# Kernel tuning notes

Hardware: AMD Instinct MI355X
Metric: run time of the kernel (lower is better)

## Reference

```python
import jax, jax.numpy as jnp
import numpy as np

B, S, HS = 2, 2048, 2048
H, HKV, D = 16, 4, 128
EPS = 1e-6
NEG = -1e9


def _rms_norm(t, w):
    t32 = t.astype(jnp.float32)
    n = t32 * jax.lax.rsqrt(jnp.mean(t32 * t32, axis=-1, keepdims=True) + EPS)
    return (w.astype(t.dtype) * n.astype(t.dtype))


def _rotate_half(x):
    x1, x2 = jnp.split(x, 2, axis=-1)
    return jnp.concatenate((-x2, x1), axis=-1)


def setup_inputs() -> dict:
    key = jax.random.key(0)
    ks = jax.random.split(key, 6)
    x = jax.random.normal(ks[0], (B, S, HS), dtype=jnp.float32)
    # RoPE tables
    inv_freq = 1.0 / (10000.0 ** (jnp.arange(0, D, 2, dtype=jnp.float32) / D))
    freqs = jnp.arange(S, dtype=jnp.float32)[:, None] * inv_freq[None, :]  # [S, D/2]
    emb = jnp.concatenate((freqs, freqs), axis=-1)  # [S, D]
    cos, sin = jnp.cos(emb), jnp.sin(emb)
    # causal additive mask [1,1,S,S]
    mask = jnp.triu(jnp.full((S, S), NEG, dtype=jnp.float32), k=1)[None, None]
    std = 0.02
    wq = jax.random.normal(ks[1], (H * D, HS), dtype=jnp.float32) * std
    wk = jax.random.normal(ks[2], (HKV * D, HS), dtype=jnp.float32) * std
    wv = jax.random.normal(ks[3], (HKV * D, HS), dtype=jnp.float32) * std
    wo = jax.random.normal(ks[4], (HS, H * D), dtype=jnp.float32) * std
    q_norm_w = jnp.ones((D,), dtype=jnp.float32)
    k_norm_w = jnp.ones((D,), dtype=jnp.float32)
    return {"x": x, "cos": cos, "sin": sin, "mask": mask,
            "wq": wq, "wk": wk, "wv": wv, "wo": wo,
            "q_norm_w": q_norm_w, "k_norm_w": k_norm_w}


def reference(x, cos, sin, mask, wq, wk, wv, wo, q_norm_w, k_norm_w):
    b, s, _ = x.shape
    n_rep = H // HKV
    scale = D ** -0.5
    # QKV projections (torch Linear: y = x @ W^T)
    q = jnp.einsum('bsh,oh->bso', x, wq).reshape(b, s, H, D).transpose(0, 2, 1, 3)
    k = jnp.einsum('bsh,oh->bso', x, wk).reshape(b, s, HKV, D).transpose(0, 2, 1, 3)
    v = jnp.einsum('bsh,oh->bso', x, wv).reshape(b, s, HKV, D).transpose(0, 2, 1, 3)
    # per-head RMS QK-norm
    q = _rms_norm(q, q_norm_w)
    k = _rms_norm(k, k_norm_w)
    # RoPE
    c = cos[None, None]
    sn = sin[None, None]
    q = q * c + _rotate_half(q) * sn
    k = k * c + _rotate_half(k) * sn
    # GQA attention without materializing repeated K/V
    qg = q.reshape(b, HKV, n_rep, s, D)
    scores = jnp.einsum('bhgqd,bhkd->bhgqk', qg, k) * scale + mask  # [b,HKV,G,S,S]
    probs = jax.nn.softmax(scores, axis=-1)
    out = jnp.einsum('bhgqk,bhkd->bhgqd', probs, v)  # [b,HKV,G,S,D]
    out = out.reshape(b, H, s, D).transpose(0, 2, 1, 3).reshape(b, s, H * D)
    return jnp.einsum('bso,ho->bsh', out, wo)
```

## Files before the change

### kernel.cpp

```cpp
#include <hip/hip_runtime.h>
#include <hip/hip_bf16.h>
#include <stdint.h>

typedef unsigned short u16;
typedef __attribute__((ext_vector_type(8))) short short8;
typedef __attribute__((ext_vector_type(4))) float f32x4;
typedef __attribute__((ext_vector_type(4))) unsigned short u16x4;

constexpr int BB = 2, SS = 2048, HSZ = 2048, NH = 16, NKV = 4, DH = 128;
constexpr int MROWS = BB * SS;
constexpr int NQKV = (NH + 2 * NKV) * DH;
constexpr float RMS_EPS = 1e-6f;

__device__ __forceinline__ u16 f2bf(float f) {
  __hip_bfloat16 h = __float2bfloat16(f);
  return *reinterpret_cast<u16*>(&h);
}
__device__ __forceinline__ float bf2f(u16 u) {
  __hip_bfloat16 h;
  *reinterpret_cast<u16*>(&h) = u;
  return __bfloat162float(h);
}

__device__ __forceinline__ void gld16(const void* g, void* l) {
  __builtin_amdgcn_global_load_lds(
      (const __attribute__((address_space(1))) void*)g,
      (__attribute__((address_space(3))) void*)l, 16, 0, 0);
}

__global__ void cvt_bf16_kernel(const float* __restrict__ in, u16* __restrict__ out, int n4) {
  int i = blockIdx.x * blockDim.x + threadIdx.x;
  if (i >= n4) return;
  float4 v = reinterpret_cast<const float4*>(in)[i];
  u16x4 o;
  o.x = f2bf(v.x); o.y = f2bf(v.y); o.z = f2bf(v.z); o.w = f2bf(v.w);
  reinterpret_cast<u16x4*>(out)[i] = o;
}

template <typename OutT>
__global__ __launch_bounds__(512, 2) void gemm256(
    const u16* __restrict__ A, const u16* __restrict__ Bm, OutT* __restrict__ C,
    int M, int N, int K, int nbn) {
  __shared__ u16 Abuf[4][256 * 32];
  __shared__ u16 Bbuf[4][256 * 32];
  const int tid = threadIdx.x;
  const int wave = tid >> 6;
  const int lane = tid & 63;
  const int nwg = gridDim.x;
  const int bid = blockIdx.x;
  const int wg = (bid & 7) * (nwg >> 3) + (bid >> 3);
  const int bm = wg / nbn, bn = wg % nbn;
  const int row0 = bm * 256, col0 = bn * 256;
  const int wm = wave >> 2, wn = wave & 3;
  const int lr = lane & 15, g = lane >> 4;
  const int sra = wave * 16 + (lane >> 2);
  const int sca = (lane & 3) * 8;
  const int lda0 = (wave * 16) * 32;
  const int lda1 = (128 + wave * 16) * 32;

  f32x4 acc[8][4] = {};
  const int nt = K / 32;

#define STAGE(T, BUFI)                                                        \
  {                                                                           \
    const int k0_ = (T) * 32;                                                 \
    u16* Ab_ = &Abuf[(BUFI)][0];                                              \
    u16* Bb_ = &Bbuf[(BUFI)][0];                                              \
    gld16(A + (size_t)(row0 + sra) * K + k0_ + sca, Ab_ + lda0);              \
    gld16(A + (size_t)(row0 + 128 + sra) * K + k0_ + sca, Ab_ + lda1);        \
    gld16(Bm + (size_t)(col0 + sra) * K + k0_ + sca, Bb_ + lda0);             \
    gld16(Bm + (size_t)(col0 + 128 + sra) * K + k0_ + sca, Bb_ + lda1);       \
  }

  STAGE(0, 0);
  STAGE(1, 1);

  for (int t = 0; t < nt; t++) {
    if (t + 2 < nt) {
      STAGE(t + 2, (t + 2) & 3);
      asm volatile("s_waitcnt vmcnt(8)" ::: "memory");
    } else if (t + 1 < nt) {
      asm volatile("s_waitcnt vmcnt(4)" ::: "memory");
    } else {
      asm volatile("s_waitcnt vmcnt(0)" ::: "memory");
    }
    __builtin_amdgcn_s_barrier();
    __builtin_amdgcn_sched_barrier(0);

    const u16* Ab = &Abuf[t & 3][0];
    const u16* Bb = &Bbuf[t & 3][0];
    short8 af[8], bfr[4];
#pragma unroll
    for (int m = 0; m < 8; m++)
      af[m] = *(const short8*)&Ab[(wm * 128 + m * 16 + lr) * 32 + g * 8];
#pragma unroll
    for (int n = 0; n < 4; n++)
      bfr[n] = *(const short8*)&Bb[(wn * 64 + n * 16 + lr) * 32 + g * 8];

    __builtin_amdgcn_s_setprio(1);
#pragma unroll
    for (int m = 0; m < 8; m++)
#pragma unroll
      for (int n = 0; n < 4; n++)
        acc[m][n] = __builtin_amdgcn_mfma_f32_16x16x32_bf16(af[m], bfr[n], acc[m][n], 0, 0, 0);
    __builtin_amdgcn_s_setprio(0);

    __builtin_amdgcn_s_barrier();
    __builtin_amdgcn_sched_barrier(0);
  }
#undef STAGE

  const int cr = g * 4, cc = lr;
#pragma unroll
  for (int m = 0; m < 8; m++) {
#pragma unroll
    for (int n = 0; n < 4; n++) {
#pragma unroll
      for (int r = 0; r < 4; r++) {
        size_t idx = (size_t)(row0 + wm * 128 + m * 16 + cr + r) * N +
                     (col0 + wn * 64 + n * 16 + cc);
        if constexpr (sizeof(OutT) == 2) C[idx] = (OutT)f2bf(acc[m][n][r]);
        else C[idx] = acc[m][n][r];
      }
    }
  }
}

__global__ __launch_bounds__(256) void postproc_kernel(
    const u16* __restrict__ Cqkv, const float* __restrict__ cosT,
    const float* __restrict__ sinT, const float* __restrict__ qw,
    const float* __restrict__ kw, u16* __restrict__ qO, u16* __restrict__ kO,
    u16* __restrict__ vO) {
  const int row = blockIdx.x;
  const int b = row / SS, s = row % SS;
  const int wave = threadIdx.x >> 6, lane = threadIdx.x & 63;
  const u16* base = Cqkv + (size_t)row * NQKV;
  const int d0 = lane * 2;
  const float ATT_SCALE = 0.08838834764831843f * 1.4426950408889634f;
  for (int hd = wave; hd < NH + 2 * NKV; hd += 4) {
    const u16* hp = base + hd * DH;
    ushort2 raw = *(const ushort2*)(hp + d0);
    if (hd < NH + NKV) {
      float v0 = bf2f(raw.x), v1 = bf2f(raw.y);
      float ss = v0 * v0 + v1 * v1;
#pragma unroll
      for (int off = 32; off > 0; off >>= 1) ss += __shfl_xor(ss, off);
      float inv = rsqrtf(ss * (1.0f / DH) + RMS_EPS);
      const float* w = (hd < NH) ? qw : kw;
      float n0 = v0 * inv * w[d0], n1 = v1 * inv * w[d0 + 1];
      float r0 = __shfl_xor(n0, 32), r1 = __shfl_xor(n1, 32);
      float sgn = (lane < 32) ? -1.f : 1.f;
      float c0 = cosT[s * DH + d0], c1 = cosT[s * DH + d0 + 1];
      float s0 = sinT[s * DH + d0], s1 = sinT[s * DH + d0 + 1];
      float o0 = n0 * c0 + sgn * r0 * s0;
      float o1 = n1 * c1 + sgn * r1 * s1;
      ushort2 o;
      if (hd < NH) {
        o.x = f2bf(o0 * ATT_SCALE);
        o.y = f2bf(o1 * ATT_SCALE);
        *(ushort2*)(qO + ((size_t)((b * NH + hd) * SS + s)) * DH + d0) = o;
      } else {
        o.x = f2bf(o0);
        o.y = f2bf(o1);
        *(ushort2*)(kO + ((size_t)((b * NKV + hd - NH) * SS + s)) * DH + d0) = o;
      }
    } else {
      *(ushort2*)(vO + ((size_t)((b * NKV + hd - NH - NKV) * SS + s)) * DH + d0) = raw;
    }
  }
}

__global__ __launch_bounds__(256) void transpose_v_kernel(const u16* __restrict__ v,
                                                          u16* __restrict__ vt) {
  __shared__ u16 tile[64][68];
  const int bh = blockIdx.z;
  const int st = blockIdx.x * 64;
  const int dt = blockIdx.y * 64;
  const int tid = threadIdx.x;
  const u16* src = v + ((size_t)bh * SS + st) * DH + dt;
#pragma unroll
  for (int it = 0; it < 4; it++) {
    int r = (tid >> 4) + it * 16, c = (tid & 15) * 4;
    *(u16x4*)&tile[r][c] = *(const u16x4*)(src + (size_t)r * DH + c);
  }
  __syncthreads();
  u16* dst = vt + ((size_t)bh * DH + dt) * SS + st;
#pragma unroll
  for (int it = 0; it < 4; it++) {
    int r2 = (tid >> 4) + it * 16, c2 = (tid & 15) * 4;
    u16x4 o;
    o.x = tile[c2][r2]; o.y = tile[c2 + 1][r2];
    o.z = tile[c2 + 2][r2]; o.w = tile[c2 + 3][r2];
    *(u16x4*)(dst + (size_t)r2 * SS + c2) = o;
  }
}

__global__ __launch_bounds__(256, 2) void attn_kernel(
    const u16* __restrict__ Q, const u16* __restrict__ Kb,
    const u16* __restrict__ Vt, u16* __restrict__ O) {
  __shared__ __align__(16) u16 Ks[64 * 128];
  __shared__ __align__(16) u16 Vs[128 * 64];
  __shared__ __align__(16) u16 Plds[4][16 * 64];
  const int pid = blockIdx.x, h = blockIdx.y, b = blockIdx.z;
  const int hkv = h >> 2;
  const int tid = threadIdx.x;
  const int wave = tid >> 6, lane = tid & 63;
  const int lr = lane & 15, g = lane >> 4;
  const u16* qbase = Q + ((size_t)(b * NH + h) * SS) * DH;
  const u16* kbase = Kb + ((size_t)(b * NKV + hkv) * SS) * DH;
  const u16* vbase = Vt + ((size_t)(b * NKV + hkv) * DH) * SS;

  const int krow = tid >> 4;
  const int kcol = (tid & 15) * 8;
  const int kswz = kcol ^ ((krow & 7) << 3);
  const int vrow = tid >> 3;
  const int vcol = (tid & 7) * 8;
  const int vswz = vcol ^ ((vrow & 7) << 3);
  const int kx = (lr & 7) << 3;
  const int psw = (lr & 7) << 4;
  char* pl = (char*)&Plds[wave][0];

  int4 kr0, kr1, kr2, kr3, vr0, vr1, vr2, vr3;
#define STAGE_LOAD(T)                                                         \
  {                                                                           \
    const int kv0_ = (T) * 64;                                                \
    kr0 = *(const int4*)(kbase + (size_t)(kv0_ + krow) * DH + kcol);          \
    kr1 = *(const int4*)(kbase + (size_t)(kv0_ + krow + 16) * DH + kcol);     \
    kr2 = *(const int4*)(kbase + (size_t)(kv0_ + krow + 32) * DH + kcol);     \
    kr3 = *(const int4*)(kbase + (size_t)(kv0_ + krow + 48) * DH + kcol);     \
    vr0 = *(const int4*)(vbase + (size_t)(vrow) * SS + kv0_ + vcol);          \
    vr1 = *(const int4*)(vbase + (size_t)(vrow + 32) * SS + kv0_ + vcol);     \
    vr2 = *(const int4*)(vbase + (size_t)(vrow + 64) * SS + kv0_ + vcol);     \
    vr3 = *(const int4*)(vbase + (size_t)(vrow + 96) * SS + kv0_ + vcol);     \
  }
#define STAGE_WRITE()                                                         \
  {                                                                           \
    *(int4*)&Ks[(krow) * DH + kswz] = kr0;                                    \
    *(int4*)&Ks[(krow + 16) * DH + kswz] = kr1;                               \
    *(int4*)&Ks[(krow + 32) * DH + kswz] = kr2;                               \
    *(int4*)&Ks[(krow + 48) * DH + kswz] = kr3;                               \
    *(int4*)&Vs[(vrow) * 64 + vswz] = vr0;                                    \
    *(int4*)&Vs[(vrow + 32) * 64 + vswz] = vr1;                               \
    *(int4*)&Vs[(vrow + 64) * 64 + vswz] = vr2;                               \
    *(int4*)&Vs[(vrow + 96) * 64 + vswz] = vr3;                               \
  }

#pragma unroll 1
  for (int half = 0; half < 2; half++) {
    const int qt = half ? (SS / 64 - 1 - pid) : pid;
    const int q0 = qt * 64 + wave * 16;
    const int nt = qt + 1;

    short8 qf[4];
#pragma unroll
    for (int c = 0; c < 4; c++)
      qf[c] = *(const short8*)(qbase + (size_t)(q0 + lr) * DH + c * 32 + g * 8);

    f32x4 o_acc[8] = {};
    float l_run = 0.f;

    STAGE_LOAD(0);
    STAGE_WRITE();
    __syncthreads();

    for (int t = 0; t < nt; t++) {
      const int kv0 = t * 64;
      if (t + 1 < nt) STAGE_LOAD(t + 1);

      f32x4 sf[4] = {};
      __builtin_amdgcn_s_setprio(1);
#pragma unroll
      for (int n = 0; n < 4; n++) {
#pragma unroll
        for (int c = 0; c < 4; c++) {
          short8 kf = *(const short8*)&Ks[(n * 16 + lr) * DH + ((c * 32 + g * 8) ^ kx)];
          sf[n] = __builtin_amdgcn_mfma_f32_16x16x32_bf16(kf, qf[c], sf[n], 0, 0, 0);
        }
      }
      __builtin_amdgcn_s_setprio(0);

      const int qabs = q0 + lr;
      float p[4][4];
      float rs = 0.f;
#pragma unroll
      for (int n = 0; n < 4; n++) {
#pragma unroll
        for (int r = 0; r < 4; r++) {
          const int kvabs = kv0 + n * 16 + g * 4 + r;
          float e = exp2f(sf[n][r] - 17.312340490667562f);
          e = (kvabs <= qabs) ? e : 0.f;
          p[n][r] = e;
          rs += e;
        }
      }
      rs += __shfl_xor(rs, 16);
      rs += __shfl_xor(rs, 32);
      l_run += rs;

#pragma unroll
      for (int n = 0; n < 4; n++) {
        uint2 wv;
        wv.x = (unsigned)f2bf(p[n][0]) | ((unsigned)f2bf(p[n][1]) << 16);
        wv.y = (unsigned)f2bf(p[n][2]) | ((unsigned)f2bf(p[n][3]) << 16);
        *(uint2*)(pl + lr * 128 + ((32 * n + 8 * g) ^ psw)) = wv;
      }

      __builtin_amdgcn_s_setprio(1);
#pragma unroll
      for (int c2 = 0; c2 < 2; c2++) {
        short8 pf = *(const short8*)(pl + lr * 128 + ((64 * c2 + 16 * g) ^ psw));
#pragma unroll
        for (int n2 = 0; n2 < 8; n2++) {
          short8 vf = *(const short8*)&Vs[(n2 * 16 + lr) * 64 + ((c2 * 32 + g * 8) ^ kx)];
          o_acc[n2] = __builtin_amdgcn_mfma_f32_16x16x32_bf16(pf, vf, o_acc[n2], 0, 0, 0);
        }
      }
      __builtin_amdgcn_s_setprio(0);

      __syncthreads();
      if (t + 1 < nt) STAGE_WRITE();
      __syncthreads();
    }

#pragma unroll
    for (int r = 0; r < 4; r++) {
      const float ls = __shfl(l_run, (g << 4) | (g * 4 + r));
      const float inv = 1.0f / ls;
      u16* orow = O + ((size_t)(b * SS + q0 + g * 4 + r)) * (NH * DH) + h * DH;
#pragma unroll
      for (int n2 = 0; n2 < 8; n2++) orow[n2 * 16 + lr] = f2bf(o_acc[n2][r] * inv);
    }
  }
#undef STAGE_LOAD
#undef STAGE_WRITE
}

extern "C" void kernel_launch(void* const* d_in, const int* in_sizes, int n_in,
                              void* d_out, int out_size, void* d_ws, size_t ws_size,
                              hipStream_t stream) {
  const float* x    = (const float*)d_in[0];
  const float* cosT = (const float*)d_in[1];
  const float* sinT = (const float*)d_in[2];
  const float* wq = (const float*)d_in[4];
  const float* wk = (const float*)d_in[5];
  const float* wv = (const float*)d_in[6];
  const float* wo = (const float*)d_in[7];
  const float* qw = (const float*)d_in[8];
  const float* kw = (const float*)d_in[9];
  float* out = (float*)d_out;

  char* p = (char*)d_ws;
  u16* xb    = (u16*)p; p += (size_t)MROWS * HSZ * 2;
  u16* wqkvb = (u16*)p; p += (size_t)NQKV * HSZ * 2;
  u16* wob   = (u16*)p; p += (size_t)HSZ * HSZ * 2;
  u16* cqkv  = (u16*)p; p += (size_t)MROWS * NQKV * 2;
  u16* qb    = (u16*)p; p += (size_t)BB * NH * SS * DH * 2;
  u16* kb    = (u16*)p; p += (size_t)BB * NKV * SS * DH * 2;
  u16* vb    = (u16*)p; p += (size_t)BB * NKV * SS * DH * 2;
  u16* vtb   = (u16*)p; p += (size_t)BB * NKV * SS * DH * 2;
  u16* aob   = (u16*)p; p += (size_t)MROWS * HSZ * 2;

  auto cvt = [&](const float* in, u16* o, size_t n) {
    int n4 = (int)(n / 4);
    cvt_bf16_kernel<<<dim3((n4 + 255) / 256), dim3(256), 0, stream>>>(in, o, n4);
  };
  cvt(x, xb, (size_t)MROWS * HSZ);
  cvt(wq, wqkvb, (size_t)NH * DH * HSZ);
  cvt(wk, wqkvb + (size_t)NH * DH * HSZ, (size_t)NKV * DH * HSZ);
  cvt(wv, wqkvb + (size_t)(NH + NKV) * DH * HSZ, (size_t)NKV * DH * HSZ);
  cvt(wo, wob, (size_t)HSZ * HSZ);

  gemm256<u16><<<dim3((MROWS / 256) * (NQKV / 256)), dim3(512), 0, stream>>>(
      xb, wqkvb, cqkv, MROWS, NQKV, HSZ, NQKV / 256);
  postproc_kernel<<<dim3(MROWS), dim3(256), 0, stream>>>(cqkv, cosT, sinT, qw, kw, qb, kb, vb);
  transpose_v_kernel<<<dim3(SS / 64, DH / 64, BB * NKV), dim3(256), 0, stream>>>(vb, vtb);
  attn_kernel<<<dim3(SS / 128, NH, BB), dim3(256), 0, stream>>>(qb, kb, vtb, aob);
  gemm256<float><<<dim3((MROWS / 256) * (HSZ / 256)), dim3(512), 0, stream>>>(
      aob, wob, out, MROWS, HSZ, HSZ, HSZ / 256);
}
```

Measured before the change: 396.0 us.

## Restructure GEMM main loop with swizzled LDS and interleaved half-tile staging; fuse conversions

Rewrites the 256x256 GEMM main loop to process two K-tiles per iteration. Each tile's MFMA work is split into two half-tile phases, and the global-to-LDS loads for A and B are interleaved between those phases. LDS rows get an XOR swizzle to avoid bank conflicts on fragment reads, and fewer A fragments are held at once, which lowers register pressure. The five separate fp32->bf16 conversion launches are merged into one kernel to cut launch overhead. In exchange the loop needs more barriers and hand-tuned waitcnt logic that is easy to get subtly wrong.

```diff
diff --git a/kernel.cpp b/kernel.cpp
--- a/kernel.cpp
+++ b/kernel.cpp
@@ -28,87 +28,152 @@
       (__attribute__((address_space(3))) void*)l, 16, 0, 0);
 }
 
-__global__ void cvt_bf16_kernel(const float* __restrict__ in, u16* __restrict__ out, int n4) {
+constexpr int N_X = MROWS * HSZ;
+constexpr int N_WQ = NH * DH * HSZ;
+constexpr int N_WK = NKV * DH * HSZ;
+constexpr int N_WO = HSZ * HSZ;
+__global__ void cvt_all_kernel(const float* __restrict__ x, const float* __restrict__ wq,
+                               const float* __restrict__ wk, const float* __restrict__ wv,
+                               const float* __restrict__ wo, u16* __restrict__ xb,
+                               u16* __restrict__ wqkvb, u16* __restrict__ wob) {
+  const int X4 = N_X / 4, Q4 = N_WQ / 4, K4 = N_WK / 4;
   int i = blockIdx.x * blockDim.x + threadIdx.x;
-  if (i >= n4) return;
-  float4 v = reinterpret_cast<const float4*>(in)[i];
+  const float* src;
+  u16* dst;
+  int off;
+  if (i < X4) { src = x; dst = xb; off = i; }
+  else if (i < X4 + Q4) { src = wq; dst = wqkvb; off = i - X4; }
+  else if (i < X4 + Q4 + K4) { src = wk; dst = wqkvb + N_WQ; off = i - X4 - Q4; }
+  else if (i < X4 + Q4 + 2 * K4) { src = wv; dst = wqkvb + N_WQ + N_WK; off = i - X4 - Q4 - K4; }
+  else { src = wo; dst = wob; off = i - X4 - Q4 - 2 * K4; }
+  float4 v = reinterpret_cast<const float4*>(src)[off];
   u16x4 o;
   o.x = f2bf(v.x); o.y = f2bf(v.y); o.z = f2bf(v.z); o.w = f2bf(v.w);
-  reinterpret_cast<u16x4*>(out)[i] = o;
+  reinterpret_cast<u16x4*>(dst)[off] = o;
 }
 
 template <typename OutT>
 __global__ __launch_bounds__(512, 2) void gemm256(
     const u16* __restrict__ A, const u16* __restrict__ Bm, OutT* __restrict__ C,
     int M, int N, int K, int nbn) {
-  __shared__ u16 Abuf[4][256 * 32];
-  __shared__ u16 Bbuf[4][256 * 32];
+  __shared__ __align__(16) u16 AS[4][256 * 32];
+  __shared__ __align__(16) u16 BS[4][256 * 32];
   const int tid = threadIdx.x;
-  const int wave = tid >> 6;
-  const int lane = tid & 63;
-  const int nwg = gridDim.x;
-  const int bid = blockIdx.x;
+  const int wave = tid >> 6, lane = tid & 63;
+  const int nwg = gridDim.x, bid = blockIdx.x;
   const int wg = (bid & 7) * (nwg >> 3) + (bid >> 3);
   const int bm = wg / nbn, bn = wg % nbn;
   const int row0 = bm * 256, col0 = bn * 256;
   const int wm = wave >> 2, wn = wave & 3;
   const int lr = lane & 15, g = lane >> 4;
-  const int sra = wave * 16 + (lane >> 2);
-  const int sca = (lane & 3) * 8;
-  const int lda0 = (wave * 16) * 32;
-  const int lda1 = (128 + wave * 16) * 32;
+
+  const int rsrc = ((tid >> 5) << 3) | ((tid & 7) ^ ((tid >> 3) & 3));
+  const int sce = ((tid >> 3) & 3) << 3;
+  const int rxor = g * 128 + (((lr & 7) ^ g) << 4);
+  const int abase = (wm * 128) << 6;
+  const int bbase = (wn * 64) << 6;
 
   f32x4 acc[8][4] = {};
-  const int nt = K / 32;
-
-#define STAGE(T, BUFI)                                                        \
-  {                                                                           \
-    const int k0_ = (T) * 32;                                                 \
-    u16* Ab_ = &Abuf[(BUFI)][0];                                              \
-    u16* Bb_ = &Bbuf[(BUFI)][0];                                              \
-    gld16(A + (size_t)(row0 + sra) * K + k0_ + sca, Ab_ + lda0);              \
-    gld16(A + (size_t)(row0 + 128 + sra) * K + k0_ + sca, Ab_ + lda1);        \
-    gld16(Bm + (size_t)(col0 + sra) * K + k0_ + sca, Bb_ + lda0);             \
-    gld16(Bm + (size_t)(col0 + 128 + sra) * K + k0_ + sca, Bb_ + lda1);       \
-  }
-
-  STAGE(0, 0);
-  STAGE(1, 1);
-
-  for (int t = 0; t < nt; t++) {
-    if (t + 2 < nt) {
-      STAGE(t + 2, (t + 2) & 3);
-      asm volatile("s_waitcnt vmcnt(8)" ::: "memory");
-    } else if (t + 1 < nt) {
-      asm volatile("s_waitcnt vmcnt(4)" ::: "memory");
-    } else {
-      asm volatile("s_waitcnt vmcnt(0)" ::: "memory");
-    }
-    __builtin_amdgcn_s_barrier();
+  const int niter = K / 64;
+
+#define STG_A(kt, sl, j)                                                      \
+  gld16(A + (size_t)(row0 + (j) * 128 + rsrc) * K + (kt) * 32 + sce,          \
+        (char*)&AS[sl][0] + (j) * 8192 + wave * 1024)
+#define STG_B(kt, sl, j)                                                      \
+  gld16(Bm + (size_t)(col0 + (j) * 128 + rsrc) * K + (kt) * 32 + sce,         \
+        (char*)&BS[sl][0] + (j) * 8192 + wave * 1024)
+
+  STG_A(0, 0, 0); STG_A(0, 0, 1); STG_B(0, 0, 0); STG_B(0, 0, 1);
+  STG_A(1, 1, 0); STG_A(1, 1, 1); STG_B(1, 1, 0); STG_B(1, 1, 1);
+  asm volatile("s_waitcnt vmcnt(4)" ::: "memory");
+  __builtin_amdgcn_s_barrier();
+
+  for (int it = 0; it < niter; it++) {
+    const bool stg = (it + 1) < niter;
+    const int slA = (2 * it) & 3, slB = (2 * it + 1) & 3;
+    const int ktS = 2 * it + 2;
+    const int ss0 = ktS & 3, ss1 = (ktS + 1) & 3;
+    const char* Ab = (const char*)&AS[slA][0];
+    const char* Bb = (const char*)&BS[slA][0];
+    short8 bf[4], af[4];
+
+#pragma unroll
+    for (int n = 0; n < 4; n++)
+      bf[n] = *(const short8*)(Bb + bbase + ((n * 16 + (lr & 8)) << 6) + rxor);
+#pragma unroll
+    for (int m = 0; m < 4; m++)
+      af[m] = *(const short8*)(Ab + abase + ((m * 16 + (lr & 8)) << 6) + rxor);
+    if (stg) { STG_A(ktS, ss0, 0); STG_A(ktS, ss0, 1); }
+    __builtin_amdgcn_s_barrier();
+    asm volatile("s_waitcnt lgkmcnt(0)" ::: "memory");
     __builtin_amdgcn_sched_barrier(0);
-
-    const u16* Ab = &Abuf[t & 3][0];
-    const u16* Bb = &Bbuf[t & 3][0];
-    short8 af[8], bfr[4];
-#pragma unroll
-    for (int m = 0; m < 8; m++)
-      af[m] = *(const short8*)&Ab[(wm * 128 + m * 16 + lr) * 32 + g * 8];
+    __builtin_amdgcn_s_setprio(1);
+#pragma unroll
+    for (int m = 0; m < 4; m++)
+#pragma unroll
+      for (int n = 0; n < 4; n++)
+        acc[m][n] = __builtin_amdgcn_mfma_f32_16x16x32_bf16(af[m], bf[n], acc[m][n], 0, 0, 0);
+    __builtin_amdgcn_s_setprio(0);
+    __builtin_amdgcn_s_barrier();
+
+#pragma unroll
+    for (int m = 0; m < 4; m++)
+      af[m] = *(const short8*)(Ab + abase + ((64 + m * 16 + (lr & 8)) << 6) + rxor);
+    if (stg) { STG_B(ktS, ss0, 0); STG_B(ktS, ss0, 1); }
+    __builtin_amdgcn_s_barrier();
+    asm volatile("s_waitcnt lgkmcnt(0)" ::: "memory");
+    __builtin_amdgcn_sched_barrier(0);
+    __builtin_amdgcn_s_setprio(1);
+#pragma unroll
+    for (int m = 0; m < 4; m++)
+#pragma unroll
+      for (int n = 0; n < 4; n++)
+        acc[4 + m][n] = __builtin_amdgcn_mfma_f32_16x16x32_bf16(af[m], bf[n], acc[4 + m][n], 0, 0, 0);
+    __builtin_amdgcn_s_setprio(0);
+    if (stg) asm volatile("s_waitcnt vmcnt(4)" ::: "memory");
+    else     asm volatile("s_waitcnt vmcnt(0)" ::: "memory");
+    __builtin_amdgcn_s_barrier();
+
+    Ab = (const char*)&AS[slB][0];
+    Bb = (const char*)&BS[slB][0];
 #pragma unroll
     for (int n = 0; n < 4; n++)
-      bfr[n] = *(const short8*)&Bb[(wn * 64 + n * 16 + lr) * 32 + g * 8];
-
+      bf[n] = *(const short8*)(Bb + bbase + ((n * 16 + (lr & 8)) << 6) + rxor);
+#pragma unroll
+    for (int m = 0; m < 4; m++)
+      af[m] = *(const short8*)(Ab + abase + ((m * 16 + (lr & 8)) << 6) + rxor);
+    if (stg) { STG_A(ktS + 1, ss1, 0); STG_A(ktS + 1, ss1, 1); }
+    __builtin_amdgcn_s_barrier();
+    asm volatile("s_waitcnt lgkmcnt(0)" ::: "memory");
+    __builtin_amdgcn_sched_barrier(0);
     __builtin_amdgcn_s_setprio(1);
 #pragma unroll
-    for (int m = 0; m < 8; m++)
+    for (int m = 0; m < 4; m++)
 #pragma unroll
       for (int n = 0; n < 4; n++)
-        acc[m][n] = __builtin_amdgcn_mfma_f32_16x16x32_bf16(af[m], bfr[n], acc[m][n], 0, 0, 0);
+        acc[m][n] = __builtin_amdgcn_mfma_f32_16x16x32_bf16(af[m], bf[n], acc[m][n], 0, 0, 0);
     __builtin_amdgcn_s_setprio(0);
-
-    __builtin_amdgcn_s_barrier();
+    __builtin_amdgcn_s_barrier();
+
+#pragma unroll
+    for (int m = 0; m < 4; m++)
+      af[m] = *(const short8*)(Ab + abase + ((64 + m * 16 + (lr & 8)) << 6) + rxor);
+    if (stg) { STG_B(ktS + 1, ss1, 0); STG_B(ktS + 1, ss1, 1); }
+    __builtin_amdgcn_s_barrier();
+    asm volatile("s_waitcnt lgkmcnt(0)" ::: "memory");
     __builtin_amdgcn_sched_barrier(0);
-  }
-#undef STAGE
+    __builtin_amdgcn_s_setprio(1);
+#pragma unroll
+    for (int m = 0; m < 4; m++)
+#pragma unroll
+      for (int n = 0; n < 4; n++)
+        acc[4 + m][n] = __builtin_amdgcn_mfma_f32_16x16x32_bf16(af[m], bf[n], acc[4 + m][n], 0, 0, 0);
+    __builtin_amdgcn_s_setprio(0);
+    if (stg) asm volatile("s_waitcnt vmcnt(4)" ::: "memory");
+    __builtin_amdgcn_s_barrier();
+  }
+#undef STG_A
+#undef STG_B
 
   const int cr = g * 4, cc = lr;
 #pragma unroll
@@ -360,15 +425,9 @@
   u16* vtb   = (u16*)p; p += (size_t)BB * NKV * SS * DH * 2;
   u16* aob   = (u16*)p; p += (size_t)MROWS * HSZ * 2;
 
-  auto cvt = [&](const float* in, u16* o, size_t n) {
-    int n4 = (int)(n / 4);
-    cvt_bf16_kernel<<<dim3((n4 + 255) / 256), dim3(256), 0, stream>>>(in, o, n4);
-  };
-  cvt(x, xb, (size_t)MROWS * HSZ);
-  cvt(wq, wqkvb, (size_t)NH * DH * HSZ);
-  cvt(wk, wqkvb + (size_t)NH * DH * HSZ, (size_t)NKV * DH * HSZ);
-  cvt(wv, wqkvb + (size_t)(NH + NKV) * DH * HSZ, (size_t)NKV * DH * HSZ);
-  cvt(wo, wob, (size_t)HSZ * HSZ);
+  const int ncvt4 = (N_X + N_WQ + 2 * N_WK + N_WO) / 4;
+  cvt_all_kernel<<<dim3(ncvt4 / 256), dim3(256), 0, stream>>>(
+      x, wq, wk, wv, wo, xb, wqkvb, wob);
 
   gemm256<u16><<<dim3((MROWS / 256) * (NQKV / 256)), dim3(512), 0, stream>>>(
       xb, wqkvb, cqkv, MROWS, NQKV, HSZ, NQKV / 256);
```

Result: faster. 366.1 us (-7.5%).
